# Optimization experiments

Measured on AMD Instinct MI355X. Metric: run time of the kernel, lower is better.

Reference implementation:

```python
import jax, jax.numpy as jnp
import numpy as np

N = 50000      # num nodes
E = 800000     # edges per hypergraph (avg degree 16)
G = 3          # hyper_edge_num
D_IN = 128
D_OUT = 128


def setup_inputs() -> dict:
    key = jax.random.key(0)
    ks = jax.random.split(key, 6)
    company_emb = jax.random.normal(ks[0], (N, D_IN), dtype=jnp.float32)
    # nn.Linear weight [out, in], glorot-ish scaling
    W = jax.random.normal(ks[1], (D_OUT, D_IN), dtype=jnp.float32) / np.sqrt(D_IN).astype(np.float32)
    alpha = jax.random.normal(ks[2], (G, 1), dtype=jnp.float32)
    edge_rows = jax.random.randint(ks[3], (G, E), 0, N, dtype=jnp.int32)
    edge_cols = jax.random.randint(ks[4], (G, E), 0, N, dtype=jnp.int32)
    edge_vals = jax.random.normal(ks[5], (G, E), dtype=jnp.float32)
    return {
        "company_emb": company_emb,
        "W": W,
        "alpha": alpha,
        "edge_rows": edge_rows,
        "edge_cols": edge_cols,
        "edge_vals": edge_vals,
    }


def reference(company_emb, W, alpha, edge_rows, edge_cols, edge_vals):
    # shared dense projection: h = X @ W^T, [N, D_OUT]
    h = company_emb @ W.T

    def spmm(rows, cols, vals):
        # sparse Laplacian (COO) @ h : gather source rows, scale, scatter-add to dest rows
        msg = vals[:, None] * h[cols]                     # [E, D_OUT]
        return jax.ops.segment_sum(msg, rows, num_segments=N)

    aggs = jax.vmap(spmm)(edge_rows, edge_cols, edge_vals)  # [G, N, D_OUT]
    gate = jax.nn.sigmoid(alpha[:, 0])                       # [G]
    # res = sum_g sigmoid(alpha_g) * (L_g @ h)
    return jnp.einsum('g,gnd->nd', gate, aggs)
```

## Files before the change

kernel.cpp:

```cpp
#include <hip/hip_runtime.h>
#include <math.h>

#define NNODES 50000
#define NEDGE  800000
#define NG     3
#define GE     (NG*NEDGE)
#define NBUK   2048
#define OS     (NBUK + 1)
#define CH     6000
#define NBLK   400
#define GBLK   391
#define FGRID  (GBLK + NBLK)
#define STGCAP 1536
#define NPH    7
#define MAXG   175
#define SCAP   2112

typedef __attribute__((ext_vector_type(8))) short bf16x8;
typedef __attribute__((ext_vector_type(4))) float f32x4;

__device__ __forceinline__ unsigned short f2bf(float f) {
    unsigned u = __float_as_uint(f);
    return (unsigned short)((u + 0x7fffu + ((u >> 16) & 1u)) >> 16);
}

__device__ __forceinline__ int bucket_of(unsigned r) {
    return (int)((r * 128u) / 3125u);
}

__global__ __launch_bounds__(512) void k_front(const float* __restrict__ X,
                                               const float* __restrict__ W,
                                               const int* __restrict__ rows,
                                               const int* __restrict__ cols,
                                               const float* __restrict__ vals,
                                               const float* __restrict__ alpha,
                                               unsigned short* __restrict__ hb16,
                                               uint2* __restrict__ out1,
                                               unsigned short* __restrict__ off1) {
    __shared__ __align__(16) char smem[34816];
    const int t = threadIdx.x;

    if (blockIdx.x < GBLK) {
        uint4* Wl = (uint4*)smem;
        for (int i = t; i < 2048; i += 512) {
            const int nt   = i >> 8;
            const int kc   = (i >> 6) & 3;
            const int lane = i & 63;
            const int n  = nt * 16 + (lane & 15);
            const int k0 = kc * 32 + (lane >> 4) * 8;
            const float* src = W + (size_t)n * 128 + k0;
            float4 a = *(const float4*)(src);
            float4 b = *(const float4*)(src + 4);
            unsigned u0 = (unsigned)f2bf(a.x) | ((unsigned)f2bf(a.y) << 16);
            unsigned u1 = (unsigned)f2bf(a.z) | ((unsigned)f2bf(a.w) << 16);
            unsigned u2 = (unsigned)f2bf(b.x) | ((unsigned)f2bf(b.y) << 16);
            unsigned u3 = (unsigned)f2bf(b.z) | ((unsigned)f2bf(b.w) << 16);
            Wl[i] = make_uint4(u0, u1, u2, u3);
        }
        __syncthreads();

        const int w    = t >> 6;
        const int lane = t & 63;
        const int q    = lane >> 4;
        const int ml   = lane & 15;
        const int m0   = blockIdx.x * 128 + w * 16;

        int xr = m0 + ml; if (xr >= NNODES) xr = NNODES - 1;
        const float* xrow = X + (size_t)xr * 128;

        bf16x8 xf[4];
#pragma unroll
        for (int kc = 0; kc < 4; ++kc) {
            const int k0 = kc * 32 + q * 8;
            float4 a = *(const float4*)(xrow + k0);
            float4 b = *(const float4*)(xrow + k0 + 4);
            bf16x8 v;
            v[0] = (short)f2bf(a.x); v[1] = (short)f2bf(a.y);
            v[2] = (short)f2bf(a.z); v[3] = (short)f2bf(a.w);
            v[4] = (short)f2bf(b.x); v[5] = (short)f2bf(b.y);
            v[6] = (short)f2bf(b.z); v[7] = (short)f2bf(b.w);
            xf[kc] = v;
        }

        f32x4 acc[8];
#pragma unroll
        for (int nt = 0; nt < 8; ++nt) acc[nt] = (f32x4){0.f, 0.f, 0.f, 0.f};
#pragma unroll
        for (int nt = 0; nt < 8; ++nt)
#pragma unroll
            for (int kc = 0; kc < 4; ++kc) {
                const bf16x8 wf = *(const bf16x8*)&Wl[(nt * 4 + kc) * 64 + lane];
                acc[nt] = __builtin_amdgcn_mfma_f32_16x16x32_bf16(xf[kc], wf, acc[nt], 0, 0, 0);
            }
        __syncthreads();

        unsigned short* hst = (unsigned short*)smem + w * 2176;
#pragma unroll
        for (int nt = 0; nt < 8; ++nt)
#pragma unroll
            for (int r = 0; r < 4; ++r)
                hst[(q * 4 + r) * 136 + nt * 16 + ml] = f2bf(acc[nt][r]);
        __syncthreads();

#pragma unroll
        for (int i = 0; i < 4; ++i) {
            const int chunk = i * 64 + lane;
            const int lr    = chunk >> 4;
            const int cc    = chunk & 15;
            const int row   = m0 + lr;
            const uint4 v = *(const uint4*)(hst + lr * 136 + cc * 8);
            if (row < NNODES)
                ((uint4*)(hb16 + (size_t)row * 128))[cc] = v;
        }
    } else {
        unsigned short* rnk = (unsigned short*)smem;
        int*            sA  = (int*)(smem + 12032);
        const int bb    = blockIdx.x - GBLK;
        const int start = bb * CH;

        const float g0 = 1.0f / (1.0f + __expf(-alpha[0]));
        const float g1 = 1.0f / (1.0f + __expf(-alpha[1]));
        const float g2 = 1.0f / (1.0f + __expf(-alpha[2]));

#pragma unroll
        for (int j = 0; j < 4; ++j) sA[t + j * 512] = 0;
        __syncthreads();

        for (int k = t; k < CH; k += 512) {
            const int r = rows[start + k];
            rnk[k] = (unsigned short)atomicAdd(&sA[bucket_of((unsigned)r)], 1);
        }
        __syncthreads();

        for (int off = 1; off < 2048; off <<= 1) {
            int v[4];
#pragma unroll
            for (int j = 0; j < 4; ++j) {
                const int i = t + j * 512;
                v[j] = sA[i] + ((i >= off) ? sA[i - off] : 0);
            }
            __syncthreads();
#pragma unroll
            for (int j = 0; j < 4; ++j) sA[t + j * 512] = v[j];
            __syncthreads();
        }

        for (int b = t; b < NBUK; b += 512)
            off1[(size_t)bb * OS + b] = (unsigned short)(b ? sA[b - 1] : 0);
        if (t == 0) off1[(size_t)bb * OS + NBUK] = (unsigned short)sA[NBUK - 1];

        for (int k = t; k < CH; k += 512) {
            const int idx = start + k;
            const int r = rows[idx];
            const int c = cols[idx];
            const float v = vals[idx];
            const float gv = v * (idx < NEDGE ? g0 : (idx < 2 * NEDGE ? g1 : g2));
            const int b = bucket_of((unsigned)r);
            const int pos = (b ? sA[b - 1] : 0) + (int)rnk[k];
            uint2 rec;
            rec.x = ((unsigned)r << 16) | (unsigned)c;
            rec.y = __float_as_uint(gv);
            out1[(size_t)bb * CH + pos] = rec;
        }
    }
}

__global__ __launch_bounds__(512, 8) void k_agg(const unsigned* __restrict__ hbits,
                                                const uint2* __restrict__ out1,
                                                const unsigned short* __restrict__ off1,
                                                float* __restrict__ out) {
    __shared__ __align__(16) uint2          stg[STGCAP];
    __shared__ __align__(16) unsigned short colS[SCAP];
    __shared__ __align__(16) float          valS[SCAP];
    __shared__ int rh[MAXG], grpBase[MAXG + 1], gcur[MAXG];
    __shared__ int sA[512];
    const int t = threadIdx.x;
    const int b = blockIdx.x;

    const int sstart = (b * 3125 + 127) >> 7;
    const int send   = ((b + 1) * 3125 + 127) >> 7;
    const int width  = send - sstart;
    const int ngrp   = NPH * width;

    if (t < MAXG) rh[t] = 0;

    int s0 = 0, e0 = 0;
    if (t < NBLK) {
        s0 = off1[(size_t)t * OS + b];
        e0 = off1[(size_t)t * OS + b + 1];
    }
    const int len = e0 - s0;
    sA[t] = len;
    __syncthreads();

    for (int off = 1; off < 512; off <<= 1) {
        const int v = sA[t] + ((t >= off) ? sA[t - off] : 0);
        __syncthreads();
        sA[t] = v;
        __syncthreads();
    }
    const int base = sA[t] - len;
    __syncthreads();

    {
        const uint2* seg = out1 + (size_t)t * CH;
        int p = base;
        for (int i = s0; i < e0; ++i, ++p) {
            const uint2 rec = seg[i];
            if (p < STGCAP) {
                stg[p] = rec;
                const int lr = (int)(rec.x >> 16) - sstart;
                const int ph = (int)((rec.x & 0xffffu) >> 13);
                atomicAdd(&rh[ph * width + lr], 1);
            }
        }
    }
    __syncthreads();

    if (t < 256) sA[t] = (t < ngrp) ? ((rh[t] + 3) & ~3) : 0;
    __syncthreads();
    for (int off = 1; off < 256; off <<= 1) {
        int v = 0;
        if (t < 256) v = sA[t] + ((t >= off) ? sA[t - off] : 0);
        __syncthreads();
        if (t < 256) sA[t] = v;
        __syncthreads();
    }
    if (t < ngrp) {
        const int pc = (rh[t] + 3) & ~3;
        const int gb = sA[t] - pc;
        grpBase[t] = gb;
        gcur[t]    = gb;
        for (int k = gb + rh[t]; k < gb + pc; ++k) { colS[k] = 0; valS[k] = 0.f; }
    }
    __syncthreads();
    if (t == 0) grpBase[ngrp] = sA[ngrp - 1];
    __syncthreads();

    {
        const int lim = (base + len < STGCAP) ? (base + len) : STGCAP;
        for (int k = base; k < lim; ++k) {
            const uint2 rec = stg[k];
            const int lr = (int)(rec.x >> 16) - sstart;
            const int ph = (int)((rec.x & 0xffffu) >> 13);
            const int pos = atomicAdd(&gcur[ph * width + lr], 1);
            colS[pos] = (unsigned short)(rec.x & 0xffffu);
            valS[pos] = __uint_as_float(rec.y);
        }
    }
    __syncthreads();

    const int w    = t >> 6;
    const int lane = t & 63;
    float2 acc[4];
#pragma unroll
    for (int ri = 0; ri < 4; ++ri) acc[ri] = make_float2(0.f, 0.f);

    for (int ph = 0; ph < NPH; ++ph) {
#pragma unroll
        for (int ri = 0; ri < 4; ++ri) {
            const int lr = w + ri * 8;
            if (lr < width) {
                const int g = ph * width + lr;
                const int s = grpBase[g];
                const int e = grpBase[g + 1];
                int i = s;
                for (; i + 8 <= e; i += 8) {
                    const uint2  ca = *(const uint2*)&colS[i];
                    const uint2  cb = *(const uint2*)&colS[i + 4];
                    const float4 v0 = *(const float4*)&valS[i];
                    const float4 v1 = *(const float4*)&valS[i + 4];
                    unsigned hb[8];
                    hb[0] = hbits[(size_t)(ca.x & 0xffffu) * 64 + lane];
                    hb[1] = hbits[(size_t)(ca.x >> 16)     * 64 + lane];
                    hb[2] = hbits[(size_t)(ca.y & 0xffffu) * 64 + lane];
                    hb[3] = hbits[(size_t)(ca.y >> 16)     * 64 + lane];
                    hb[4] = hbits[(size_t)(cb.x & 0xffffu) * 64 + lane];
                    hb[5] = hbits[(size_t)(cb.x >> 16)     * 64 + lane];
                    hb[6] = hbits[(size_t)(cb.y & 0xffffu) * 64 + lane];
                    hb[7] = hbits[(size_t)(cb.y >> 16)     * 64 + lane];
                    const float vv[8] = {v0.x, v0.y, v0.z, v0.w, v1.x, v1.y, v1.z, v1.w};
#pragma unroll
                    for (int j = 0; j < 8; ++j) {
                        acc[ri].x += vv[j] * __uint_as_float(hb[j] << 16);
                        acc[ri].y += vv[j] * __uint_as_float(hb[j] & 0xffff0000u);
                    }
                }
                if (i < e) {
                    const uint2  ca = *(const uint2*)&colS[i];
                    const float4 v0 = *(const float4*)&valS[i];
                    unsigned hb[4];
                    hb[0] = hbits[(size_t)(ca.x & 0xffffu) * 64 + lane];
                    hb[1] = hbits[(size_t)(ca.x >> 16)     * 64 + lane];
                    hb[2] = hbits[(size_t)(ca.y & 0xffffu) * 64 + lane];
                    hb[3] = hbits[(size_t)(ca.y >> 16)     * 64 + lane];
                    const float vv[4] = {v0.x, v0.y, v0.z, v0.w};
#pragma unroll
                    for (int j = 0; j < 4; ++j) {
                        acc[ri].x += vv[j] * __uint_as_float(hb[j] << 16);
                        acc[ri].y += vv[j] * __uint_as_float(hb[j] & 0xffff0000u);
                    }
                }
            }
        }
    }

#pragma unroll
    for (int ri = 0; ri < 4; ++ri) {
        const int lr = w + ri * 8;
        if (lr < width) {
            const int row = sstart + lr;
            ((float2*)out)[(size_t)row * 64 + lane] = acc[ri];
        }
    }
}

extern "C" void kernel_launch(void* const* d_in, const int* in_sizes, int n_in,
                              void* d_out, int out_size, void* d_ws, size_t ws_size,
                              hipStream_t stream) {
    const float* X     = (const float*)d_in[0];
    const float* W     = (const float*)d_in[1];
    const float* alpha = (const float*)d_in[2];
    const int*   rows  = (const int*)d_in[3];
    const int*   cols  = (const int*)d_in[4];
    const float* vals  = (const float*)d_in[5];
    float* out = (float*)d_out;

    char* ws = (char*)d_ws;
    unsigned*       hbits = (unsigned*)(ws + 0);
    unsigned short* hb16  = (unsigned short*)(ws + 0);
    uint2*          out1  = (uint2*)(ws + 12800000);
    unsigned short* off1  = (unsigned short*)(ws + 32000000);

    hipLaunchKernelGGL(k_front, dim3(FGRID), dim3(512), 0, stream,
                       X, W, rows, cols, vals, alpha, hb16, out1, off1);
    hipLaunchKernelGGL(k_agg, dim3(NBUK), dim3(512), 0, stream,
                       hbits, out1, off1, out);
}
```

Baseline: 212.5 us.

## Split fused front kernel into separate weight-prep, binning and GEMM kernels

The heterogeneous front kernel, which ran GEMM blocks and edge-binning blocks in one grid, is split into three launches. A single-block kernel converts W to a bf16 MFMA fragment layout once in global memory, the binning kernel runs alone, and the GEMM kernel then copies the pre-packed W into LDS instead of converting it in every block. This removes the per-block W conversion and lets each kernel use its own LDS footprint, at the cost of two extra launches, a serialized one-block prep kernel, and the loss of overlap between GEMM and binning work.

New measurement: 232.6 us. 9.4% more time.

```diff
diff --git a/kernel.cpp b/kernel.cpp
--- a/kernel.cpp
+++ b/kernel.cpp
@@ -10,7 +10,6 @@
 #define CH     6000
 #define NBLK   400
 #define GBLK   391
-#define FGRID  (GBLK + NBLK)
 #define STGCAP 1536
 #define NPH    7
 #define MAXG   175
@@ -28,140 +27,143 @@
     return (int)((r * 128u) / 3125u);
 }
 
-__global__ __launch_bounds__(512) void k_front(const float* __restrict__ X,
-                                               const float* __restrict__ W,
-                                               const int* __restrict__ rows,
-                                               const int* __restrict__ cols,
-                                               const float* __restrict__ vals,
-                                               const float* __restrict__ alpha,
-                                               unsigned short* __restrict__ hb16,
-                                               uint2* __restrict__ out1,
-                                               unsigned short* __restrict__ off1) {
+__global__ void k_wprep(const float* __restrict__ W, uint4* __restrict__ Wf) {
+    const int t = threadIdx.x;
+    for (int i = t; i < 2048; i += 256) {
+        const int nt   = i >> 8;
+        const int kc   = (i >> 6) & 3;
+        const int lane = i & 63;
+        const int n  = nt * 16 + (lane & 15);
+        const int k0 = kc * 32 + (lane >> 4) * 8;
+        const float* src = W + (size_t)n * 128 + k0;
+        unsigned u0 = (unsigned)f2bf(src[0]) | ((unsigned)f2bf(src[1]) << 16);
+        unsigned u1 = (unsigned)f2bf(src[2]) | ((unsigned)f2bf(src[3]) << 16);
+        unsigned u2 = (unsigned)f2bf(src[4]) | ((unsigned)f2bf(src[5]) << 16);
+        unsigned u3 = (unsigned)f2bf(src[6]) | ((unsigned)f2bf(src[7]) << 16);
+        Wf[i] = make_uint4(u0, u1, u2, u3);
+    }
+}
+
+__global__ __launch_bounds__(512) void k_gemm(const float* __restrict__ X,
+                                              const uint4* __restrict__ Wf,
+                                              unsigned short* __restrict__ hb16) {
     __shared__ __align__(16) char smem[34816];
     const int t = threadIdx.x;
-
-    if (blockIdx.x < GBLK) {
-        uint4* Wl = (uint4*)smem;
-        for (int i = t; i < 2048; i += 512) {
-            const int nt   = i >> 8;
-            const int kc   = (i >> 6) & 3;
-            const int lane = i & 63;
-            const int n  = nt * 16 + (lane & 15);
-            const int k0 = kc * 32 + (lane >> 4) * 8;
-            const float* src = W + (size_t)n * 128 + k0;
-            float4 a = *(const float4*)(src);
-            float4 b = *(const float4*)(src + 4);
-            unsigned u0 = (unsigned)f2bf(a.x) | ((unsigned)f2bf(a.y) << 16);
-            unsigned u1 = (unsigned)f2bf(a.z) | ((unsigned)f2bf(a.w) << 16);
-            unsigned u2 = (unsigned)f2bf(b.x) | ((unsigned)f2bf(b.y) << 16);
-            unsigned u3 = (unsigned)f2bf(b.z) | ((unsigned)f2bf(b.w) << 16);
-            Wl[i] = make_uint4(u0, u1, u2, u3);
-        }
-        __syncthreads();
-
-        const int w    = t >> 6;
-        const int lane = t & 63;
-        const int q    = lane >> 4;
-        const int ml   = lane & 15;
-        const int m0   = blockIdx.x * 128 + w * 16;
-
-        int xr = m0 + ml; if (xr >= NNODES) xr = NNODES - 1;
-        const float* xrow = X + (size_t)xr * 128;
-
-        bf16x8 xf[4];
+    uint4* Wl = (uint4*)smem;
+#pragma unroll
+    for (int j = 0; j < 4; ++j) Wl[t + j * 512] = Wf[t + j * 512];
+    __syncthreads();
+
+    const int w    = t >> 6;
+    const int lane = t & 63;
+    const int q    = lane >> 4;
+    const int ml   = lane & 15;
+    const int m0   = blockIdx.x * 128 + w * 16;
+
+    int xr = m0 + ml; if (xr >= NNODES) xr = NNODES - 1;
+    const float* xrow = X + (size_t)xr * 128;
+
+    bf16x8 xf[4];
+#pragma unroll
+    for (int kc = 0; kc < 4; ++kc) {
+        const int k0 = kc * 32 + q * 8;
+        float4 a = *(const float4*)(xrow + k0);
+        float4 b = *(const float4*)(xrow + k0 + 4);
+        bf16x8 v;
+        v[0] = (short)f2bf(a.x); v[1] = (short)f2bf(a.y);
+        v[2] = (short)f2bf(a.z); v[3] = (short)f2bf(a.w);
+        v[4] = (short)f2bf(b.x); v[5] = (short)f2bf(b.y);
+        v[6] = (short)f2bf(b.z); v[7] = (short)f2bf(b.w);
+        xf[kc] = v;
+    }
+
+    f32x4 acc[8];
+#pragma unroll
+    for (int nt = 0; nt < 8; ++nt) acc[nt] = (f32x4){0.f, 0.f, 0.f, 0.f};
+#pragma unroll
+    for (int nt = 0; nt < 8; ++nt)
 #pragma unroll
         for (int kc = 0; kc < 4; ++kc) {
-            const int k0 = kc * 32 + q * 8;
-            float4 a = *(const float4*)(xrow + k0);
-            float4 b = *(const float4*)(xrow + k0 + 4);
-            bf16x8 v;
-            v[0] = (short)f2bf(a.x); v[1] = (short)f2bf(a.y);
-            v[2] = (short)f2bf(a.z); v[3] = (short)f2bf(a.w);
-            v[4] = (short)f2bf(b.x); v[5] = (short)f2bf(b.y);
-            v[6] = (short)f2bf(b.z); v[7] = (short)f2bf(b.w);
-            xf[kc] = v;
-        }
-
-        f32x4 acc[8];
-#pragma unroll
-        for (int nt = 0; nt < 8; ++nt) acc[nt] = (f32x4){0.f, 0.f, 0.f, 0.f};
-#pragma unroll
-        for (int nt = 0; nt < 8; ++nt)
-#pragma unroll
-            for (int kc = 0; kc < 4; ++kc) {
-                const bf16x8 wf = *(const bf16x8*)&Wl[(nt * 4 + kc) * 64 + lane];
-                acc[nt] = __builtin_amdgcn_mfma_f32_16x16x32_bf16(xf[kc], wf, acc[nt], 0, 0, 0);
-            }
-        __syncthreads();
-
-        unsigned short* hst = (unsigned short*)smem + w * 2176;
-#pragma unroll
-        for (int nt = 0; nt < 8; ++nt)
-#pragma unroll
-            for (int r = 0; r < 4; ++r)
-                hst[(q * 4 + r) * 136 + nt * 16 + ml] = f2bf(acc[nt][r]);
-        __syncthreads();
-
-#pragma unroll
-        for (int i = 0; i < 4; ++i) {
-            const int chunk = i * 64 + lane;
-            const int lr    = chunk >> 4;
-            const int cc    = chunk & 15;
-            const int row   = m0 + lr;
-            const uint4 v = *(const uint4*)(hst + lr * 136 + cc * 8);
-            if (row < NNODES)
-                ((uint4*)(hb16 + (size_t)row * 128))[cc] = v;
-        }
-    } else {
-        unsigned short* rnk = (unsigned short*)smem;
-        int*            sA  = (int*)(smem + 12032);
-        const int bb    = blockIdx.x - GBLK;
-        const int start = bb * CH;
-
-        const float g0 = 1.0f / (1.0f + __expf(-alpha[0]));
-        const float g1 = 1.0f / (1.0f + __expf(-alpha[1]));
-        const float g2 = 1.0f / (1.0f + __expf(-alpha[2]));
-
-#pragma unroll
-        for (int j = 0; j < 4; ++j) sA[t + j * 512] = 0;
-        __syncthreads();
-
-        for (int k = t; k < CH; k += 512) {
-            const int r = rows[start + k];
-            rnk[k] = (unsigned short)atomicAdd(&sA[bucket_of((unsigned)r)], 1);
-        }
-        __syncthreads();
-
-        for (int off = 1; off < 2048; off <<= 1) {
-            int v[4];
-#pragma unroll
-            for (int j = 0; j < 4; ++j) {
-                const int i = t + j * 512;
-                v[j] = sA[i] + ((i >= off) ? sA[i - off] : 0);
-            }
-            __syncthreads();
-#pragma unroll
-            for (int j = 0; j < 4; ++j) sA[t + j * 512] = v[j];
-            __syncthreads();
-        }
-
-        for (int b = t; b < NBUK; b += 512)
-            off1[(size_t)bb * OS + b] = (unsigned short)(b ? sA[b - 1] : 0);
-        if (t == 0) off1[(size_t)bb * OS + NBUK] = (unsigned short)sA[NBUK - 1];
-
-        for (int k = t; k < CH; k += 512) {
-            const int idx = start + k;
-            const int r = rows[idx];
-            const int c = cols[idx];
-            const float v = vals[idx];
-            const float gv = v * (idx < NEDGE ? g0 : (idx < 2 * NEDGE ? g1 : g2));
-            const int b = bucket_of((unsigned)r);
-            const int pos = (b ? sA[b - 1] : 0) + (int)rnk[k];
-            uint2 rec;
-            rec.x = ((unsigned)r << 16) | (unsigned)c;
-            rec.y = __float_as_uint(gv);
-            out1[(size_t)bb * CH + pos] = rec;
-        }
+            const bf16x8 wf = *(const bf16x8*)&Wl[(nt * 4 + kc) * 64 + lane];
+            acc[nt] = __builtin_amdgcn_mfma_f32_16x16x32_bf16(xf[kc], wf, acc[nt], 0, 0, 0);
+        }
+    __syncthreads();
+
+    unsigned short* hst = (unsigned short*)smem + w * 2176;
+#pragma unroll
+    for (int nt = 0; nt < 8; ++nt)
+#pragma unroll
+        for (int r = 0; r < 4; ++r)
+            hst[(q * 4 + r) * 136 + nt * 16 + ml] = f2bf(acc[nt][r]);
+    __syncthreads();
+
+#pragma unroll
+    for (int i = 0; i < 4; ++i) {
+        const int chunk = i * 64 + lane;
+        const int lr    = chunk >> 4;
+        const int cc    = chunk & 15;
+        const int row   = m0 + lr;
+        const uint4 v = *(const uint4*)(hst + lr * 136 + cc * 8);
+        if (row < NNODES)
+            ((uint4*)(hb16 + (size_t)row * 128))[cc] = v;
+    }
+}
+
+__global__ __launch_bounds__(512) void k_bin(const int* __restrict__ rows,
+                                             const int* __restrict__ cols,
+                                             const float* __restrict__ vals,
+                                             const float* __restrict__ alpha,
+                                             uint2* __restrict__ out1,
+                                             unsigned short* __restrict__ off1) {
+    __shared__ unsigned short rnk[CH];
+    __shared__ int sA[NBUK];
+    const int t     = threadIdx.x;
+    const int bb    = blockIdx.x;
+    const int start = bb * CH;
+
+    const float g0 = 1.0f / (1.0f + __expf(-alpha[0]));
+    const float g1 = 1.0f / (1.0f + __expf(-alpha[1]));
+    const float g2 = 1.0f / (1.0f + __expf(-alpha[2]));
+
+#pragma unroll
+    for (int j = 0; j < 4; ++j) sA[t + j * 512] = 0;
+    __syncthreads();
+
+    for (int k = t; k < CH; k += 512) {
+        const int r = rows[start + k];
+        rnk[k] = (unsigned short)atomicAdd(&sA[bucket_of((unsigned)r)], 1);
+    }
+    __syncthreads();
+
+    for (int off = 1; off < 2048; off <<= 1) {
+        int v[4];
+#pragma unroll
+        for (int j = 0; j < 4; ++j) {
+            const int i = t + j * 512;
+            v[j] = sA[i] + ((i >= off) ? sA[i - off] : 0);
+        }
+        __syncthreads();
+#pragma unroll
+        for (int j = 0; j < 4; ++j) sA[t + j * 512] = v[j];
+        __syncthreads();
+    }
+
+    for (int b = t; b < NBUK; b += 512)
+        off1[(size_t)bb * OS + b] = (unsigned short)(b ? sA[b - 1] : 0);
+    if (t == 0) off1[(size_t)bb * OS + NBUK] = (unsigned short)sA[NBUK - 1];
+
+    for (int k = t; k < CH; k += 512) {
+        const int idx = start + k;
+        const int r = rows[idx];
+        const int c = cols[idx];
+        const float v = vals[idx];
+        const float gv = v * (idx < NEDGE ? g0 : (idx < 2 * NEDGE ? g1 : g2));
+        const int b = bucket_of((unsigned)r);
+        const int pos = (b ? sA[b - 1] : 0) + (int)rnk[k];
+        uint2 rec;
+        rec.x = ((unsigned)r << 16) | (unsigned)c;
+        rec.y = __float_as_uint(gv);
+        out1[(size_t)bb * CH + pos] = rec;
     }
 }
 
@@ -331,9 +333,12 @@
     unsigned short* hb16  = (unsigned short*)(ws + 0);
     uint2*          out1  = (uint2*)(ws + 12800000);
     unsigned short* off1  = (unsigned short*)(ws + 32000000);
-
-    hipLaunchKernelGGL(k_front, dim3(FGRID), dim3(512), 0, stream,
-                       X, W, rows, cols, vals, alpha, hb16, out1, off1);
+    uint4*          Wf    = (uint4*)(ws + 33639200);
+
+    hipLaunchKernelGGL(k_wprep, dim3(1), dim3(256), 0, stream, W, Wf);
+    hipLaunchKernelGGL(k_bin, dim3(NBLK), dim3(512), 0, stream,
+                       rows, cols, vals, alpha, out1, off1);
+    hipLaunchKernelGGL(k_gemm, dim3(GBLK), dim3(512), 0, stream, X, Wf, hb16);
     hipLaunchKernelGGL(k_agg, dim3(NBUK), dim3(512), 0, stream,
                        hbits, out1, off1, out);
 }
```

## Use fewer, larger edge chunks and split each segment read across two threads

Applied to the files above, without the earlier changes.

The bucketing phase now runs 256 blocks of 9375 edges instead of 400 blocks of 6000, so each gather block reads 256 segments. Each segment is split between two threads (halves), so all 512 threads copy records into staging. This cuts per-thread serial segment walking and the number of offset loads. Gather address computation switches from 64-bit size_t multiplies to 32-bit shift/or indexing to trim address arithmetic. Larger chunks add shared-memory use for the rank array and leave fewer blocks in the first phase.

Result: slower. 217.1 us (+2.2%).

```diff
diff --git a/kernel.cpp b/kernel.cpp
--- a/kernel.cpp
+++ b/kernel.cpp
@@ -7,8 +7,8 @@
 #define GE     (NG*NEDGE)
 #define NBUK   2048
 #define OS     (NBUK + 1)
-#define CH     6000
-#define NBLK   400
+#define CH     9375
+#define NBLK   256
 #define GBLK   391
 #define FGRID  (GBLK + NBLK)
 #define STGCAP 1536
@@ -114,7 +114,7 @@
         }
     } else {
         unsigned short* rnk = (unsigned short*)smem;
-        int*            sA  = (int*)(smem + 12032);
+        int*            sA  = (int*)(smem + 18752);
         const int bb    = blockIdx.x - GBLK;
         const int start = bb * CH;
 
@@ -184,12 +184,15 @@
 
     if (t < MAXG) rh[t] = 0;
 
-    int s0 = 0, e0 = 0;
-    if (t < NBLK) {
-        s0 = off1[(size_t)t * OS + b];
-        e0 = off1[(size_t)t * OS + b + 1];
-    }
-    const int len = e0 - s0;
+    const int seg  = t & 255;
+    const int s0f  = off1[(size_t)seg * OS + b];
+    const int e0f  = off1[(size_t)seg * OS + b + 1];
+    const int lenf = e0f - s0f;
+    const int mid  = s0f + ((lenf + 1) >> 1);
+    const int half = t >> 8;
+    const int s0   = half ? mid : s0f;
+    const int e0   = half ? e0f : mid;
+    const int len  = e0 - s0;
     sA[t] = len;
     __syncthreads();
 
@@ -203,10 +206,10 @@
     __syncthreads();
 
     {
-        const uint2* seg = out1 + (size_t)t * CH;
+        const uint2* segp = out1 + (size_t)seg * CH;
         int p = base;
         for (int i = s0; i < e0; ++i, ++p) {
-            const uint2 rec = seg[i];
+            const uint2 rec = segp[i];
             if (p < STGCAP) {
                 stg[p] = rec;
                 const int lr = (int)(rec.x >> 16) - sstart;
@@ -252,6 +255,7 @@
 
     const int w    = t >> 6;
     const int lane = t & 63;
+#define GATH(cc) hbits[(((unsigned)(cc)) << 6) | (unsigned)lane]
     float2 acc[4];
 #pragma unroll
     for (int ri = 0; ri < 4; ++ri) acc[ri] = make_float2(0.f, 0.f);
@@ -271,14 +275,14 @@
                     const float4 v0 = *(const float4*)&valS[i];
                     const float4 v1 = *(const float4*)&valS[i + 4];
                     unsigned hb[8];
-                    hb[0] = hbits[(size_t)(ca.x & 0xffffu) * 64 + lane];
-                    hb[1] = hbits[(size_t)(ca.x >> 16)     * 64 + lane];
-                    hb[2] = hbits[(size_t)(ca.y & 0xffffu) * 64 + lane];
-                    hb[3] = hbits[(size_t)(ca.y >> 16)     * 64 + lane];
-                    hb[4] = hbits[(size_t)(cb.x & 0xffffu) * 64 + lane];
-                    hb[5] = hbits[(size_t)(cb.x >> 16)     * 64 + lane];
-                    hb[6] = hbits[(size_t)(cb.y & 0xffffu) * 64 + lane];
-                    hb[7] = hbits[(size_t)(cb.y >> 16)     * 64 + lane];
+                    hb[0] = GATH(ca.x & 0xffffu);
+                    hb[1] = GATH(ca.x >> 16);
+                    hb[2] = GATH(ca.y & 0xffffu);
+                    hb[3] = GATH(ca.y >> 16);
+                    hb[4] = GATH(cb.x & 0xffffu);
+                    hb[5] = GATH(cb.x >> 16);
+                    hb[6] = GATH(cb.y & 0xffffu);
+                    hb[7] = GATH(cb.y >> 16);
                     const float vv[8] = {v0.x, v0.y, v0.z, v0.w, v1.x, v1.y, v1.z, v1.w};
 #pragma unroll
                     for (int j = 0; j < 8; ++j) {
@@ -290,10 +294,10 @@
                     const uint2  ca = *(const uint2*)&colS[i];
                     const float4 v0 = *(const float4*)&valS[i];
                     unsigned hb[4];
-                    hb[0] = hbits[(size_t)(ca.x & 0xffffu) * 64 + lane];
-                    hb[1] = hbits[(size_t)(ca.x >> 16)     * 64 + lane];
-                    hb[2] = hbits[(size_t)(ca.y & 0xffffu) * 64 + lane];
-                    hb[3] = hbits[(size_t)(ca.y >> 16)     * 64 + lane];
+                    hb[0] = GATH(ca.x & 0xffffu);
+                    hb[1] = GATH(ca.x >> 16);
+                    hb[2] = GATH(ca.y & 0xffffu);
+                    hb[3] = GATH(ca.y >> 16);
                     const float vv[4] = {v0.x, v0.y, v0.z, v0.w};
 #pragma unroll
                     for (int j = 0; j < 4; ++j) {
@@ -304,6 +308,7 @@
             }
         }
     }
+#undef GATH
 
 #pragma unroll
     for (int ri = 0; ri < 4; ++ri) {
```
